# Kernel tuning notes

Hardware: AMD Instinct MI355X
Metric: run time of the kernel (lower is better)

The kernel has to match this reference:

```python
import jax, jax.numpy as jnp
import numpy as np

N, D, A, K, E = 8192, 256, 1024, 65, 4096

def setup_inputs() -> dict:
    key = jax.random.key(0)
    ks = jax.random.split(key, 8)
    s = 0.02  # linear-init scale to keep activations sane
    return {
        "embedding": jax.random.normal(ks[0], (N, D), jnp.float32),
        "data": jax.random.randint(ks[1], (E, 2), 0, N, jnp.int64),
        "Wq": jax.random.normal(ks[2], (D, A), jnp.float32) * s,
        "bq": jnp.zeros((A,), jnp.float32),
        "Wk": jax.random.normal(ks[3], (D, A), jnp.float32) * s,
        "bk": jnp.zeros((A,), jnp.float32),
        "Wv": jax.random.normal(ks[4], (D, A), jnp.float32) * s,
        "bv": jnp.zeros((A,), jnp.float32),
        "W_edge": jax.random.normal(ks[5], (K, A, A), jnp.float32) * s,
    }

def reference(embedding, data, Wq, bq, Wk, bk, Wv, bv, W_edge):
    # NodeSelfAttention: dense full attention over all N nodes
    Q = embedding @ Wq + bq            # [N, A]
    Km = embedding @ Wk + bk           # [N, A]
    V = embedding @ Wv + bv            # [N, A]
    scale = 1.0 / jnp.sqrt(jnp.float32(D))  # note: sqrt(num_feats)=sqrt(256), as in source
    scores = (Q @ Km.T) * scale        # [N, N]
    attn = jax.nn.softmax(scores, axis=-1)
    attn_emb = attn @ V                # [N, A]
    # gather edge endpoints
    h_u = attn_emb[data[:, 0]]         # [E, A]
    h_v = attn_emb[data[:, 1]]         # [E, A]
    # KWayPred: out[e,k] = h_u[e] @ W_edge[k] @ h_v[e]
    # (source computes full ExE matmul per k and takes diag; this is the
    #  equivalent O(E*K*A^2) bilinear-diag form)
    t = jnp.einsum('ed,kdf->ekf', h_u, W_edge)   # [E, K, A]
    out = jnp.einsum('ekf,ef->ek', t, h_v)       # [E, K]
    return out
```

## Files before the change

kernel.cpp:

```cpp
#include <hip/hip_runtime.h>
#include <cstdio>
#include <cstdint>

#define NTOK 8192
#define DIM  256
#define AA   1024
#define KE   65
#define EE   4096

typedef unsigned short u16;
typedef __attribute__((ext_vector_type(4))) float   f32x4;
typedef __attribute__((ext_vector_type(8))) short   bf16x8;
typedef __attribute__((ext_vector_type(8))) unsigned short u16x8;

#define DEVI __device__ __forceinline__

DEVI u16 f2bf(float f) {
  union { float f; unsigned u; } x; x.f = f;
  unsigned r = x.u + 0x7FFFu + ((x.u >> 16) & 1u);
  return (u16)(r >> 16);
}
DEVI float bf2f(u16 h) {
  union { unsigned u; float f; } x; x.u = ((unsigned)h) << 16;
  return x.f;
}

DEVI void gload16(const void* g, void* l) {
  __builtin_amdgcn_global_load_lds(
      (const __attribute__((address_space(1))) void*)g,
      (__attribute__((address_space(3))) void*)l,
      16, 0, 0);
}

DEVI void barx() {
  asm volatile("" ::: "memory");
  __builtin_amdgcn_s_barrier();
  asm volatile("" ::: "memory");
}

DEVI void stage_half(const u16* __restrict__ g0, int ld, char* dst, int tid) {
#pragma unroll
  for (int rr = 0; rr < 2; ++rr) {
    int o = rr * 8192 + (tid >> 6) * 1024 + (tid & 63) * 16;
    int q = o ^ (((o >> 7) & 7) << 4);
    gload16(g0 + (size_t)(q >> 7) * ld + ((q & 127) >> 1),
            dst + rr * 8192 + (tid >> 6) * 1024);
  }
}

template<int EPI, int QMODE>
__global__ __launch_bounds__(512, 2)
void gemm8(const u16* __restrict__ A, int lda,
           const u16* __restrict__ B, int ldb,
           int MT, int NT, int K,
           u16* __restrict__ o_s, float scale, int ldc,
           const u16* __restrict__ Hu, float* __restrict__ o_e,
           int* __restrict__ qcnt)
{
  __shared__ __align__(16) char lds[131072];
  __shared__ int s_idx;
  char* ldsA = lds;
  char* ldsB = lds + 65536;

  const int tid = threadIdx.x, lane = tid & 63, wave = tid >> 6;
  const int wm = (wave >> 2) * 128;
  const int wn = (wave & 3) * 64;
  const int wnl = (wave & 1) * 64;
  const int KT = K >> 6, KT2 = KT >> 1;
  const int r15 = lane & 15, g16 = (lane >> 4) << 4;

  int xcc;
  asm volatile("s_getreg_b32 %0, hwreg(20, 0, 32)" : "=s"(xcc));
  xcc &= 7;
  const int MPX = MT >> 3;
  const int NQ = NT >> 3, NR = NT & 7;

  const char* Ab_e = ldsA +         (wm >> 7) * 16384;
  const char* Ab_o = ldsA + 32768 + (wm >> 7) * 16384;
  const char* Bb_e = ldsB +         (wn >> 7) * 16384;
  const char* Bb_o = ldsB + 32768 + (wn >> 7) * 16384;

#define STAGE_A(tk, h) stage_half(A + (size_t)(m0 + (h)*128) * lda + (size_t)(tk)*64, lda, \
                                  ldsA + ((tk)&1) * 32768 + (h) * 16384, tid)
#define STAGE_B(tk, h) stage_half(B + (size_t)(n0 + (h)*128) * ldb + (size_t)(tk)*64, ldb, \
                                  ldsB + ((tk)&1) * 32768 + (h) * 16384, tid)
#define RD_A4(base, q) \
  _Pragma("unroll") for (int m = (q)*4; m < (q)*4+4; ++m) \
  _Pragma("unroll") for (int kk = 0; kk < 2; ++kk) { \
    int p = (m*16 + r15)*128 + kk*64 + g16; p ^= ((p>>7)&7)<<4; \
    a[m][kk] = *(const bf16x8*)((base) + p); }
#define RD_B2(base, q) \
  _Pragma("unroll") for (int n = (q)*2; n < (q)*2+2; ++n) \
  _Pragma("unroll") for (int kk = 0; kk < 2; ++kk) { \
    int p = (wnl + n*16 + r15)*128 + kk*64 + g16; p ^= ((p>>7)&7)<<4; \
    b[n][kk] = *(const bf16x8*)((base) + p); }
#define MM(QM, QN) do { \
  __builtin_amdgcn_s_setprio(1); \
  _Pragma("unroll") for (int kk = 0; kk < 2; ++kk) \
  _Pragma("unroll") for (int m = 0; m < 4; ++m) \
  _Pragma("unroll") for (int n = 0; n < 2; ++n) \
    acc[(QM)*4+m][(QN)*2+n] = __builtin_amdgcn_mfma_f32_16x16x32_bf16( \
        a[(QM)*4+m][kk], b[(QN)*2+n][kk], acc[(QM)*4+m][(QN)*2+n], 0, 0, 0); \
  __builtin_amdgcn_s_setprio(0); } while (0)
#define WAIT_LGKM0 do { asm volatile("s_waitcnt lgkmcnt(0)" ::: "memory"); \
                        __builtin_amdgcn_sched_barrier(0); } while (0)

  for (int dx = 0; dx < 8; ++dx) {
    const int qi = (xcc + dx) & 7;
    int per, nt_base = 0, nt_cnt = 0;
    if constexpr (QMODE == 0) {
      per = (MT * NT) >> 3;
    } else {
      nt_cnt  = NQ + (qi < NR ? 1 : 0);
      nt_base = qi * NQ + (qi < NR ? qi : NR);
      per     = nt_cnt * MT;
    }
    while (true) {
      if (tid == 0) s_idx = atomicAdd(&qcnt[qi], 1);
      __syncthreads();
      const int idx = s_idx;
      __syncthreads();
      if (idx >= per) break;
      int mt, nt;
      if constexpr (QMODE == 0) {
        mt = qi * MPX + (idx % MPX);
        nt = idx / MPX;
      } else {
        const int srw = nt_cnt << 3;
        const int sr  = idx / srw;
        const int rem = idx - sr * srw;
        nt = nt_base + (rem >> 3);
        mt = (sr << 3) + (rem & 7);
      }
      const int m0 = mt * 256, n0 = nt * 256;

      f32x4 acc[8][4];
#pragma unroll
      for (int m = 0; m < 8; ++m)
#pragma unroll
        for (int n = 0; n < 4; ++n) acc[m][n] = f32x4{0.f, 0.f, 0.f, 0.f};

      STAGE_A(0, 0); STAGE_A(0, 1); STAGE_B(0, 0); STAGE_B(0, 1);
      STAGE_A(1, 0); STAGE_B(1, 0);
      asm volatile("s_waitcnt vmcnt(4)" ::: "memory");
      barx();

      for (int i = 0; i < KT2; ++i) {
        const int ta = 2 * i, tb = 2 * i + 1;
        const bool lastI = (i == KT2 - 1);
        bf16x8 a[8][2], b[4][2];

        RD_B2(Bb_e, 0); RD_A4(Ab_e, 0);
        STAGE_A(tb, 1);
        asm volatile("s_waitcnt lgkmcnt(8)" ::: "memory");
        barx(); WAIT_LGKM0;
        MM(0, 0);
        barx();
        RD_B2(Bb_e, 1);
        STAGE_B(tb, 1);
        barx(); WAIT_LGKM0;
        MM(0, 1);
        barx();
        RD_A4(Ab_e, 1);
        if (!lastI) STAGE_B(ta + 2, 0);
        barx(); WAIT_LGKM0;
        MM(1, 1);
        barx();
        if (!lastI) STAGE_A(ta + 2, 0);
        barx();
        __builtin_amdgcn_sched_barrier(0);
        MM(1, 0);
        if (!lastI) asm volatile("s_waitcnt vmcnt(4)" ::: "memory");
        else        asm volatile("s_waitcnt vmcnt(0)" ::: "memory");
        barx();

        RD_B2(Bb_o, 0); RD_A4(Ab_o, 0);
        if (!lastI) STAGE_A(ta + 2, 1);
        asm volatile("s_waitcnt lgkmcnt(8)" ::: "memory");
        barx(); WAIT_LGKM0;
        MM(0, 0);
        barx();
        RD_B2(Bb_o, 1);
        if (!lastI) STAGE_B(ta + 2, 1);
        barx(); WAIT_LGKM0;
        MM(0, 1);
        barx();
        RD_A4(Ab_o, 1);
        if (!lastI) STAGE_B(tb + 2, 0);
        barx(); WAIT_LGKM0;
        MM(1, 1);
        barx();
        if (!lastI) STAGE_A(tb + 2, 0);
        barx();
        __builtin_amdgcn_sched_barrier(0);
        MM(1, 0);
        if (!lastI) asm volatile("s_waitcnt vmcnt(4)" ::: "memory");
        else        asm volatile("s_waitcnt vmcnt(0)" ::: "memory");
        barx();
      }

      const int rgrp = lane >> 4, cid = lane & 15;
      if constexpr (EPI == 1) {
#pragma unroll
        for (int m = 0; m < 8; ++m)
#pragma unroll
          for (int n = 0; n < 4; ++n)
#pragma unroll
            for (int j = 0; j < 4; ++j) {
              int row = m0 + wm + m * 16 + rgrp * 4 + j;
              int col = n0 + wn + n * 16 + cid;
              o_s[(size_t)row * ldc + col] = f2bf(acc[m][n][j] * scale);
            }
      } else {
        const int kidx  = n0 >> 10;
        const int dbase = (n0 & 1023) + wn;
#pragma unroll
        for (int m = 0; m < 8; ++m)
#pragma unroll
          for (int j = 0; j < 4; ++j) {
            int row = m0 + wm + m * 16 + rgrp * 4 + j;
            float p = 0.f;
#pragma unroll
            for (int n = 0; n < 4; ++n)
              p += acc[m][n][j] * bf2f(Hu[(size_t)row * AA + dbase + n * 16 + cid]);
            p += __shfl_xor(p, 1, 64);
            p += __shfl_xor(p, 2, 64);
            p += __shfl_xor(p, 4, 64);
            p += __shfl_xor(p, 8, 64);
            if (cid == 0) atomicAdd(&o_e[(size_t)row * KE + kidx], p);
          }
      }
    }
  }
#undef STAGE_A
#undef STAGE_B
#undef RD_A4
#undef RD_B2
#undef MM
#undef WAIT_LGKM0
}

#define BM 128
#define BN 128
#define BK 64

template<int EPI, bool BF32>
__global__ __launch_bounds__(256)
void gemm_bt(const u16* __restrict__ A, int lda,
             const void* __restrict__ Bptr, int ldb,
             int MT, int NT, int K,
             u16* __restrict__ o_q, u16* __restrict__ o_k, u16* __restrict__ o_vt,
             const float* __restrict__ biasc,
             u16* __restrict__ o_s, float scale, int ldc,
             const u16* __restrict__ Hu, float* __restrict__ o_e)
{
  const int nb  = MT * NT;
  const int per = nb >> 3;
  int bid = blockIdx.x;
  bid = (bid & 7) * per + (bid >> 3);
  const int mt = bid % MT, nt = bid / MT;
  const int m0 = mt * BM, n0 = nt * BN;

  __shared__ u16 As[BM * BK];
  __shared__ u16 Bs[BN * BK];

  const int tid  = threadIdx.x;
  const int lane = tid & 63, wave = tid >> 6;
  const int wm = (wave >> 1) * 64, wn = (wave & 1) * 64;

  f32x4 acc[4][4];
#pragma unroll
  for (int m = 0; m < 4; ++m)
#pragma unroll
    for (int n = 0; n < 4; ++n) acc[m][n] = f32x4{0.f, 0.f, 0.f, 0.f};

  const u16*   Bh = (const u16*)Bptr;
  const float* Bf = (const float*)Bptr;

  const int KT = K / BK;
  for (int kt = 0; kt < KT; ++kt) {
    const int k0 = kt * BK;
#pragma unroll
    for (int it = 0; it < 4; ++it) {
      int o = it * 4096 + wave * 1024 + lane * 16;
      int r = o >> 7;
      int c = (o & 127) >> 1;
      gload16(A + (size_t)(m0 + r) * lda + k0 + c,
              &As[(it * 4096 + wave * 1024) >> 1]);
    }
    if constexpr (!BF32) {
#pragma unroll
      for (int it = 0; it < 4; ++it) {
        int o = it * 4096 + wave * 1024 + lane * 16;
        int r = o >> 7;
        int c = (o & 127) >> 1;
        gload16(Bh + (size_t)(n0 + r) * ldb + k0 + c,
                &Bs[(it * 4096 + wave * 1024) >> 1]);
      }
    } else {
#pragma unroll
      for (int it = 0; it < 8; ++it) {
        int e = it * 1024 + tid * 4;
        int r = e >> 6, c = e & 63;
        const float4 v = *(const float4*)(Bf + (size_t)(n0 + r) * ldb + k0 + c);
        ushort4 h;
        h.x = f2bf(v.x); h.y = f2bf(v.y); h.z = f2bf(v.z); h.w = f2bf(v.w);
        *(ushort4*)&Bs[r * BK + c] = h;
      }
    }
    asm volatile("s_waitcnt vmcnt(0)" ::: "memory");
    __syncthreads();

#pragma unroll
    for (int kk = 0; kk < 2; ++kk) {
      const int ro = lane & 15;
      const int ko = kk * 32 + (lane >> 4) * 8;
      bf16x8 af[4], bfg[4];
#pragma unroll
      for (int m = 0; m < 4; ++m)
        af[m] = *(const bf16x8*)&As[(wm + m * 16 + ro) * BK + ko];
#pragma unroll
      for (int n = 0; n < 4; ++n)
        bfg[n] = *(const bf16x8*)&Bs[(wn + n * 16 + ro) * BK + ko];
#pragma unroll
      for (int m = 0; m < 4; ++m)
#pragma unroll
        for (int n = 0; n < 4; ++n)
          acc[m][n] = __builtin_amdgcn_mfma_f32_16x16x32_bf16(
              af[m], bfg[n], acc[m][n], 0, 0, 0);
    }
    __syncthreads();
  }

  const int rgrp = lane >> 4, cid = lane & 15;

  if constexpr (EPI == 0) {
#pragma unroll
    for (int m = 0; m < 4; ++m)
#pragma unroll
      for (int n = 0; n < 4; ++n)
#pragma unroll
        for (int j = 0; j < 4; ++j) {
          int row = m0 + wm + m * 16 + rgrp * 4 + j;
          int col = n0 + wn + n * 16 + cid;
          float v = acc[m][n][j] + biasc[col];
          u16 h = f2bf(v);
          if (col < 1024)       o_q[(size_t)row * AA + col] = h;
          else if (col < 2048)  o_k[(size_t)row * AA + (col - 1024)] = h;
          else                  o_vt[(size_t)(col - 2048) * NTOK + row] = h;
        }
  } else if constexpr (EPI == 1) {
#pragma unroll
    for (int m = 0; m < 4; ++m)
#pragma unroll
      for (int n = 0; n < 4; ++n)
#pragma unroll
        for (int j = 0; j < 4; ++j) {
          int row = m0 + wm + m * 16 + rgrp * 4 + j;
          int col = n0 + wn + n * 16 + cid;
          o_s[(size_t)row * ldc + col] = f2bf(acc[m][n][j] * scale);
        }
  } else {
    const int kidx  = n0 >> 10;
    const int dbase = (n0 & 1023) + wn;
#pragma unroll
    for (int m = 0; m < 4; ++m)
#pragma unroll
      for (int j = 0; j < 4; ++j) {
        int row = m0 + wm + m * 16 + rgrp * 4 + j;
        float p = 0.f;
#pragma unroll
        for (int n = 0; n < 4; ++n) {
          int d = dbase + n * 16 + cid;
          p += acc[m][n][j] * bf2f(Hu[(size_t)row * AA + d]);
        }
        p += __shfl_xor(p, 1, 64);
        p += __shfl_xor(p, 2, 64);
        p += __shfl_xor(p, 4, 64);
        p += __shfl_xor(p, 8, 64);
        if (cid == 0) atomicAdd(&o_e[(size_t)row * KE + kidx], p);
      }
  }
}

__global__ __launch_bounds__(256)
void softmax_rows(u16* __restrict__ S)
{
  const size_t base = (size_t)blockIdx.x * 8192;
  const int tid = threadIdx.x;
  const int lane = tid & 63, wave = tid >> 6;
  float v[32];
#pragma unroll
  for (int c = 0; c < 4; ++c) {
    u16x8 u = *(const u16x8*)&S[base + c * 2048 + tid * 8];
#pragma unroll
    for (int j = 0; j < 8; ++j) v[c * 8 + j] = bf2f(u[j]);
  }
  float mx = -1e30f;
#pragma unroll
  for (int i = 0; i < 32; ++i) mx = fmaxf(mx, v[i]);
#pragma unroll
  for (int off = 1; off < 64; off <<= 1) mx = fmaxf(mx, __shfl_xor(mx, off, 64));
  __shared__ float r1[4], r2[4];
  if (lane == 0) r1[wave] = mx;
  __syncthreads();
  mx = fmaxf(fmaxf(r1[0], r1[1]), fmaxf(r1[2], r1[3]));

  float s = 0.f;
#pragma unroll
  for (int i = 0; i < 32; ++i) { v[i] = __expf(v[i] - mx); s += v[i]; }
#pragma unroll
  for (int off = 1; off < 64; off <<= 1) s += __shfl_xor(s, off, 64);
  if (lane == 0) r2[wave] = s;
  __syncthreads();
  s = r2[0] + r2[1] + r2[2] + r2[3];
  const float inv = 1.f / s;
#pragma unroll
  for (int c = 0; c < 4; ++c) {
    u16x8 u;
#pragma unroll
    for (int j = 0; j < 8; ++j) u[j] = f2bf(v[c * 8 + j] * inv);
    *(u16x8*)&S[base + c * 2048 + tid * 8] = u;
  }
}

__global__ __launch_bounds__(256)
void gather_rows(const unsigned* __restrict__ dw, const u16* __restrict__ AE,
                 u16* __restrict__ Hu, u16* __restrict__ Hv)
{
  bool i64 = true;
#pragma unroll
  for (int w = 1; w < 32; w += 2) i64 = i64 && (dw[w] == 0u);
  const int e = blockIdx.x;
  const unsigned iu = i64 ? dw[4 * e]     : dw[2 * e];
  const unsigned iv = i64 ? dw[4 * e + 2] : dw[2 * e + 1];
  const int t = threadIdx.x;
  *(ushort4*)&Hu[(size_t)e * AA + t * 4] = *(const ushort4*)&AE[(size_t)iu * AA + t * 4];
  *(ushort4*)&Hv[(size_t)e * AA + t * 4] = *(const ushort4*)&AE[(size_t)iv * AA + t * 4];
}

__global__ __launch_bounds__(256)
void init_misc(float* __restrict__ out_e, const float* __restrict__ bq,
               const float* __restrict__ bk, const float* __restrict__ bv,
               float* __restrict__ biasc, int* __restrict__ qall)
{
  const int i = blockIdx.x * 256 + threadIdx.x;
  if (i < EE * KE) out_e[i] = 0.f;
  if (i < 1024) {
    biasc[i]        = bq[i];
    biasc[1024 + i] = bk[i];
    biasc[2048 + i] = bv[i];
  }
  if (i < 24) qall[i] = 0;
}

__global__ __launch_bounds__(256)
void cvt_f32_bf16_v4(const float* __restrict__ src, u16* __restrict__ dst, int n4)
{
  for (int i = blockIdx.x * 256 + threadIdx.x; i < n4; i += gridDim.x * 256) {
    float4 v = ((const float4*)src)[i];
    ushort4 h; h.x = f2bf(v.x); h.y = f2bf(v.y); h.z = f2bf(v.z); h.w = f2bf(v.w);
    ((ushort4*)dst)[i] = h;
  }
}

__global__ __launch_bounds__(256)
void build_wT(const float* __restrict__ Wq, const float* __restrict__ Wk,
              const float* __restrict__ Wv, u16* __restrict__ WT)
{
  const int nn = blockIdx.x;
  const int d  = threadIdx.x;
  const float* W = (nn < 1024) ? Wq : ((nn < 2048) ? Wk : Wv);
  WT[nn * DIM + d] = f2bf(W[(size_t)d * AA + (nn & 1023)]);
}

extern "C" void kernel_launch(void* const* d_in, const int* in_sizes, int n_in,
                              void* d_out, int out_size, void* d_ws, size_t ws_size,
                              hipStream_t stream)
{
  (void)in_sizes; (void)out_size;
  if (n_in < 9) return;
  const float*    emb  = (const float*)d_in[0];
  const unsigned* data = (const unsigned*)d_in[1];
  const float* Wq = (const float*)d_in[2];
  const float* bq = (const float*)d_in[3];
  const float* Wk = (const float*)d_in[4];
  const float* bk = (const float*)d_in[5];
  const float* Wv = (const float*)d_in[6];
  const float* bv = (const float*)d_in[7];
  const float* We = (const float*)d_in[8];
  float* out = (float*)d_out;

  char* ws = (char*)d_ws;
  size_t off = 0;
  auto alloc = [&](size_t bytes) -> void* {
    void* p = ws + off;
    off += (bytes + 255) & ~(size_t)255;
    return p;
  };
  u16*   emb_b = (u16*)alloc((size_t)NTOK * DIM * 2);
  u16*   WT    = (u16*)alloc((size_t)3072 * DIM * 2);
  float* biasc = (float*)alloc(3072 * 4);
  int*   qall  = (int*)alloc(24 * 4);
  u16*   Qb    = (u16*)alloc((size_t)NTOK * AA * 2);
  u16*   Kb    = (u16*)alloc((size_t)NTOK * AA * 2);
  u16*   Vt    = (u16*)alloc((size_t)AA * NTOK * 2);
  u16*   AE    = (u16*)alloc((size_t)NTOK * AA * 2);
  u16*   Hu    = (u16*)alloc((size_t)EE * AA * 2);
  u16*   Hv    = (u16*)alloc((size_t)EE * AA * 2);

  const size_t webf_bytes = ((size_t)KE * AA * AA * 2 + 255) & ~(size_t)255;
  u16* We_b = nullptr;
  if (off + webf_bytes + (size_t)1024 * NTOK * 2 <= ws_size) {
    We_b = (u16*)(ws + off);
    off += webf_bytes;
  }

  int chunk = 4096;
  while (chunk > 128 && off + (size_t)chunk * NTOK * 2 > ws_size) chunk >>= 1;
  u16* Sc = (u16*)alloc((size_t)chunk * NTOK * 2);
  if (off > ws_size) {
    fprintf(stderr, "kernel_launch: ws too small (need %zu, have %zu)\n", off, ws_size);
    return;
  }

  init_misc<<<(EE * KE) / 256, 256, 0, stream>>>(out, bq, bk, bv, biasc, qall);
  cvt_f32_bf16_v4<<<2048, 256, 0, stream>>>(emb, emb_b, NTOK * DIM / 4);
  build_wT<<<3072, 256, 0, stream>>>(Wq, Wk, Wv, WT);
  if (We_b)
    cvt_f32_bf16_v4<<<4096, 256, 0, stream>>>(We, We_b, KE * AA * AA / 4);

  gemm_bt<0, false><<<64 * 24, 256, 0, stream>>>(
      emb_b, DIM, WT, DIM, 64, 24, DIM,
      Qb, Kb, Vt, biasc, nullptr, 0.f, 0, nullptr, nullptr);

  const int nch = NTOK / chunk;
  for (int ci = 0; ci < nch; ++ci) {
    const u16* Qc = Qb + (size_t)ci * chunk * AA;
    if ((chunk & 2047) == 0)
      gemm8<1, 1><<<256, 512, 0, stream>>>(
          Qc, AA, Kb, AA, chunk / 256, 32, AA,
          Sc, 0.0625f, NTOK, nullptr, nullptr, qall + 8 * (ci & 1));
    else
      gemm_bt<1, false><<<(chunk / 128) * 64, 256, 0, stream>>>(
          Qc, AA, Kb, AA, chunk / 128, 64, AA,
          nullptr, nullptr, nullptr, nullptr, Sc, 0.0625f, NTOK, nullptr, nullptr);
    softmax_rows<<<chunk, 256, 0, stream>>>(Sc);
    gemm_bt<1, false><<<(chunk / 128) * 8, 256, 0, stream>>>(
        Sc, NTOK, Vt, NTOK, chunk / 128, 8, NTOK,
        nullptr, nullptr, nullptr, nullptr,
        AE + (size_t)ci * chunk * AA, 1.0f, AA, nullptr, nullptr);
  }

  gather_rows<<<EE, 256, 0, stream>>>(data, AE, Hu, Hv);

  if (We_b)
    gemm8<2, 1><<<256, 512, 0, stream>>>(
        Hv, AA, We_b, AA, 16, 260, AA,
        nullptr, 0.f, 0, Hu, out, qall + 16);
  else
    gemm_bt<3, true><<<32 * 520, 256, 0, stream>>>(
        Hv, AA, We, AA, 32, 520, AA,
        nullptr, nullptr, nullptr, nullptr, nullptr, 0.f, 0, Hu, out);
}
```

Before: 1.729 ms.

## Prefetch next tile across persistent gemm8 tiles and use gemm8 for attn@V

The persistent gemm8 kernel now pops its next tile index early, during the second-to-last K iteration, and starts staging that tile's first K slices while the current tile finishes. This removes the prologue bubble and the double __syncthreads between tiles. The K loop is restructured into a KTILE macro with deeper prefetch (vmcnt 6). The attn@V GEMM also switches from gemm_bt to gemm8 when the chunk is big, using QMODE 0, which needs separate queue counters per chunk. The cost is a more complex pipeline, with a risk of LDS races and higher register pressure.

Result: faster. 1.620 ms (-6.3%).

```diff
diff --git a/kernel.cpp b/kernel.cpp
--- a/kernel.cpp
+++ b/kernel.cpp
@@ -58,7 +58,7 @@
            int* __restrict__ qcnt)
 {
   __shared__ __align__(16) char lds[131072];
-  __shared__ int s_idx;
+  __shared__ int s_next[3];
   char* ldsA = lds;
   char* ldsB = lds + 65536;
 
@@ -80,10 +80,51 @@
   const char* Bb_e = ldsB +         (wn >> 7) * 16384;
   const char* Bb_o = ldsB + 32768 + (wn >> 7) * 16384;
 
-#define STAGE_A(tk, h) stage_half(A + (size_t)(m0 + (h)*128) * lda + (size_t)(tk)*64, lda, \
-                                  ldsA + ((tk)&1) * 32768 + (h) * 16384, tid)
-#define STAGE_B(tk, h) stage_half(B + (size_t)(n0 + (h)*128) * ldb + (size_t)(tk)*64, ldb, \
-                                  ldsB + ((tk)&1) * 32768 + (h) * 16384, tid)
+  int dxr = 0;
+  auto pop_next = [&]() {
+    while (dxr < 8) {
+      const int qi = (xcc + dxr) & 7;
+      int per, ntb = 0, ntc = 0;
+      if constexpr (QMODE == 0) {
+        per = (MT * NT) >> 3;
+      } else {
+        ntc = NQ + (qi < NR ? 1 : 0);
+        ntb = qi * NQ + (qi < NR ? qi : NR);
+        per = ntc * MT;
+      }
+      const int idx = atomicAdd(&qcnt[qi], 1);
+      if (idx < per) {
+        int mt, nt;
+        if constexpr (QMODE == 0) {
+          mt = qi * MPX + (idx % MPX); nt = idx / MPX;
+        } else {
+          const int srw = ntc << 3;
+          const int sr = idx / srw, rem = idx - sr * srw;
+          nt = ntb + (rem >> 3); mt = (sr << 3) + (rem & 7);
+        }
+        s_next[0] = mt * 256; s_next[1] = nt * 256; s_next[2] = 1;
+        return;
+      }
+      ++dxr;
+    }
+    s_next[2] = 0;
+  };
+
+  if (tid == 0) pop_next();
+  __syncthreads();
+  int m0 = s_next[0], n0 = s_next[1];
+  if (!s_next[2]) return;
+
+#define STAGE_A2(tk, h) do { const int _tk = (tk); \
+    if (_tk < KT) stage_half(A + (size_t)(m0 + (h)*128) * lda + (size_t)_tk*64, lda, \
+                             ldsA + (_tk & 1) * 32768 + (h) * 16384, tid); \
+    else if (have_n) stage_half(A + (size_t)(m0n + (h)*128) * lda + (size_t)(_tk-KT)*64, lda, \
+                                ldsA + (_tk & 1) * 32768 + (h) * 16384, tid); } while (0)
+#define STAGE_B2(tk, h) do { const int _tk = (tk); \
+    if (_tk < KT) stage_half(B + (size_t)(n0 + (h)*128) * ldb + (size_t)_tk*64, ldb, \
+                             ldsB + (_tk & 1) * 32768 + (h) * 16384, tid); \
+    else if (have_n) stage_half(B + (size_t)(n0n + (h)*128) * ldb + (size_t)(_tk-KT)*64, ldb, \
+                                ldsB + (_tk & 1) * 32768 + (h) * 16384, tid); } while (0)
 #define RD_A4(base, q) \
   _Pragma("unroll") for (int m = (q)*4; m < (q)*4+4; ++m) \
   _Pragma("unroll") for (int kk = 0; kk < 2; ++kk) { \
@@ -104,140 +145,106 @@
   __builtin_amdgcn_s_setprio(0); } while (0)
 #define WAIT_LGKM0 do { asm volatile("s_waitcnt lgkmcnt(0)" ::: "memory"); \
                         __builtin_amdgcn_sched_barrier(0); } while (0)
-
-  for (int dx = 0; dx < 8; ++dx) {
-    const int qi = (xcc + dx) & 7;
-    int per, nt_base = 0, nt_cnt = 0;
-    if constexpr (QMODE == 0) {
-      per = (MT * NT) >> 3;
-    } else {
-      nt_cnt  = NQ + (qi < NR ? 1 : 0);
-      nt_base = qi * NQ + (qi < NR ? qi : NR);
-      per     = nt_cnt * MT;
+#define KTILE(t, AB, BB) do { \
+     \
+    RD_B2(BB, 0); RD_A4(AB, 0); \
+    STAGE_B2((t) + 1, 1); \
+    asm volatile("s_waitcnt lgkmcnt(8)" ::: "memory"); \
+    barx(); WAIT_LGKM0; \
+    MM(0, 0); \
+    barx(); \
+     \
+    RD_B2(BB, 1); \
+    barx(); WAIT_LGKM0; \
+    MM(0, 1); \
+    barx(); \
+     \
+    RD_A4(AB, 1); \
+    STAGE_B2((t) + 2, 0); \
+    barx(); WAIT_LGKM0; \
+    MM(1, 1); \
+    barx(); \
+     \
+    STAGE_A2((t) + 2, 0); \
+    STAGE_A2((t) + 2, 1); \
+    barx(); \
+    __builtin_amdgcn_sched_barrier(0); \
+    MM(1, 0); \
+    if (vm6) asm volatile("s_waitcnt vmcnt(6)" ::: "memory"); \
+    else     asm volatile("s_waitcnt vmcnt(0)" ::: "memory"); \
+    barx(); } while (0)
+
+  {
+    const int m0n = 0, n0n = 0; const bool have_n = false; (void)m0n; (void)n0n; (void)have_n;
+    STAGE_A2(0, 0); STAGE_A2(0, 1); STAGE_B2(0, 0); STAGE_B2(0, 1);
+    STAGE_B2(1, 0); STAGE_A2(1, 0); STAGE_A2(1, 1);
+  }
+  asm volatile("s_waitcnt vmcnt(6)" ::: "memory");
+  barx();
+
+  while (true) {
+    f32x4 acc[8][4];
+#pragma unroll
+    for (int m = 0; m < 8; ++m)
+#pragma unroll
+      for (int n = 0; n < 4; ++n) acc[m][n] = f32x4{0.f, 0.f, 0.f, 0.f};
+
+    int m0n = 0, n0n = 0;
+    bool have_n = false;
+
+    for (int i = 0; i < KT2; ++i) {
+      const int ta = 2 * i, tb = 2 * i + 1;
+      if (i == KT2 - 2 && tid == 0) pop_next();
+      if (i == KT2 - 1) { m0n = s_next[0]; n0n = s_next[1]; have_n = (s_next[2] != 0); }
+      const bool tail = (i == KT2 - 1);
+      const bool vm6 = !tail || have_n;
+      bf16x8 a[8][2], b[4][2];
+      KTILE(ta, Ab_e, Bb_e);
+      KTILE(tb, Ab_o, Bb_o);
     }
-    while (true) {
-      if (tid == 0) s_idx = atomicAdd(&qcnt[qi], 1);
-      __syncthreads();
-      const int idx = s_idx;
-      __syncthreads();
-      if (idx >= per) break;
-      int mt, nt;
-      if constexpr (QMODE == 0) {
-        mt = qi * MPX + (idx % MPX);
-        nt = idx / MPX;
-      } else {
-        const int srw = nt_cnt << 3;
-        const int sr  = idx / srw;
-        const int rem = idx - sr * srw;
-        nt = nt_base + (rem >> 3);
-        mt = (sr << 3) + (rem & 7);
-      }
-      const int m0 = mt * 256, n0 = nt * 256;
-
-      f32x4 acc[8][4];
+
+    const int rgrp = lane >> 4, cid = lane & 15;
+    if constexpr (EPI == 1) {
 #pragma unroll
       for (int m = 0; m < 8; ++m)
 #pragma unroll
-        for (int n = 0; n < 4; ++n) acc[m][n] = f32x4{0.f, 0.f, 0.f, 0.f};
-
-      STAGE_A(0, 0); STAGE_A(0, 1); STAGE_B(0, 0); STAGE_B(0, 1);
-      STAGE_A(1, 0); STAGE_B(1, 0);
-      asm volatile("s_waitcnt vmcnt(4)" ::: "memory");
-      barx();
-
-      for (int i = 0; i < KT2; ++i) {
-        const int ta = 2 * i, tb = 2 * i + 1;
-        const bool lastI = (i == KT2 - 1);
-        bf16x8 a[8][2], b[4][2];
-
-        RD_B2(Bb_e, 0); RD_A4(Ab_e, 0);
-        STAGE_A(tb, 1);
-        asm volatile("s_waitcnt lgkmcnt(8)" ::: "memory");
-        barx(); WAIT_LGKM0;
-        MM(0, 0);
-        barx();
-        RD_B2(Bb_e, 1);
-        STAGE_B(tb, 1);
-        barx(); WAIT_LGKM0;
-        MM(0, 1);
-        barx();
-        RD_A4(Ab_e, 1);
-        if (!lastI) STAGE_B(ta + 2, 0);
-        barx(); WAIT_LGKM0;
-        MM(1, 1);
-        barx();
-        if (!lastI) STAGE_A(ta + 2, 0);
-        barx();
-        __builtin_amdgcn_sched_barrier(0);
-        MM(1, 0);
-        if (!lastI) asm volatile("s_waitcnt vmcnt(4)" ::: "memory");
-        else        asm volatile("s_waitcnt vmcnt(0)" ::: "memory");
-        barx();
-
-        RD_B2(Bb_o, 0); RD_A4(Ab_o, 0);
-        if (!lastI) STAGE_A(ta + 2, 1);
-        asm volatile("s_waitcnt lgkmcnt(8)" ::: "memory");
-        barx(); WAIT_LGKM0;
-        MM(0, 0);
-        barx();
-        RD_B2(Bb_o, 1);
-        if (!lastI) STAGE_B(ta + 2, 1);
-        barx(); WAIT_LGKM0;
-        MM(0, 1);
-        barx();
-        RD_A4(Ab_o, 1);
-        if (!lastI) STAGE_B(tb + 2, 0);
-        barx(); WAIT_LGKM0;
-        MM(1, 1);
-        barx();
-        if (!lastI) STAGE_A(tb + 2, 0);
-        barx();
-        __builtin_amdgcn_sched_barrier(0);
-        MM(1, 0);
-        if (!lastI) asm volatile("s_waitcnt vmcnt(4)" ::: "memory");
-        else        asm volatile("s_waitcnt vmcnt(0)" ::: "memory");
-        barx();
-      }
-
-      const int rgrp = lane >> 4, cid = lane & 15;
-      if constexpr (EPI == 1) {
-#pragma unroll
-        for (int m = 0; m < 8; ++m)
-#pragma unroll
-          for (int n = 0; n < 4; ++n)
-#pragma unroll
-            for (int j = 0; j < 4; ++j) {
-              int row = m0 + wm + m * 16 + rgrp * 4 + j;
-              int col = n0 + wn + n * 16 + cid;
-              o_s[(size_t)row * ldc + col] = f2bf(acc[m][n][j] * scale);
-            }
-      } else {
-        const int kidx  = n0 >> 10;
-        const int dbase = (n0 & 1023) + wn;
-#pragma unroll
-        for (int m = 0; m < 8; ++m)
+        for (int n = 0; n < 4; ++n)
 #pragma unroll
           for (int j = 0; j < 4; ++j) {
             int row = m0 + wm + m * 16 + rgrp * 4 + j;
-            float p = 0.f;
-#pragma unroll
-            for (int n = 0; n < 4; ++n)
-              p += acc[m][n][j] * bf2f(Hu[(size_t)row * AA + dbase + n * 16 + cid]);
-            p += __shfl_xor(p, 1, 64);
-            p += __shfl_xor(p, 2, 64);
-            p += __shfl_xor(p, 4, 64);
-            p += __shfl_xor(p, 8, 64);
-            if (cid == 0) atomicAdd(&o_e[(size_t)row * KE + kidx], p);
+            int col = n0 + wn + n * 16 + cid;
+            o_s[(size_t)row * ldc + col] = f2bf(acc[m][n][j] * scale);
           }
-      }
+    } else {
+      const int kidx  = n0 >> 10;
+      const int dbase = (n0 & 1023) + wn;
+#pragma unroll
+      for (int m = 0; m < 8; ++m)
+#pragma unroll
+        for (int j = 0; j < 4; ++j) {
+          int row = m0 + wm + m * 16 + rgrp * 4 + j;
+          float p = 0.f;
+#pragma unroll
+          for (int n = 0; n < 4; ++n)
+            p += acc[m][n][j] * bf2f(Hu[(size_t)row * AA + dbase + n * 16 + cid]);
+          p += __shfl_xor(p, 1, 64);
+          p += __shfl_xor(p, 2, 64);
+          p += __shfl_xor(p, 4, 64);
+          p += __shfl_xor(p, 8, 64);
+          if (cid == 0) atomicAdd(&o_e[(size_t)row * KE + kidx], p);
+        }
     }
-  }
-#undef STAGE_A
-#undef STAGE_B
+
+    if (!have_n) break;
+    m0 = m0n; n0 = n0n;
+  }
+#undef STAGE_A2
+#undef STAGE_B2
 #undef RD_A4
 #undef RD_B2
 #undef MM
 #undef WAIT_LGKM0
+#undef KTILE
 }
 
 #define BM 128
@@ -451,7 +458,7 @@
     biasc[1024 + i] = bk[i];
     biasc[2048 + i] = bv[i];
   }
-  if (i < 24) qall[i] = 0;
+  if (i < 64) qall[i] = 0;
 }
 
 __global__ __launch_bounds__(256)
@@ -501,7 +508,7 @@
   u16*   emb_b = (u16*)alloc((size_t)NTOK * DIM * 2);
   u16*   WT    = (u16*)alloc((size_t)3072 * DIM * 2);
   float* biasc = (float*)alloc(3072 * 4);
-  int*   qall  = (int*)alloc(24 * 4);
+  int*   qall  = (int*)alloc(64 * 4);
   u16*   Qb    = (u16*)alloc((size_t)NTOK * AA * 2);
   u16*   Kb    = (u16*)alloc((size_t)NTOK * AA * 2);
   u16*   Vt    = (u16*)alloc((size_t)AA * NTOK * 2);
@@ -537,19 +544,25 @@
   const int nch = NTOK / chunk;
   for (int ci = 0; ci < nch; ++ci) {
     const u16* Qc = Qb + (size_t)ci * chunk * AA;
-    if ((chunk & 2047) == 0)
+    const bool big = ((chunk & 2047) == 0);
+    if (big)
       gemm8<1, 1><<<256, 512, 0, stream>>>(
           Qc, AA, Kb, AA, chunk / 256, 32, AA,
-          Sc, 0.0625f, NTOK, nullptr, nullptr, qall + 8 * (ci & 1));
+          Sc, 0.0625f, NTOK, nullptr, nullptr, qall + 8 * ci);
     else
       gemm_bt<1, false><<<(chunk / 128) * 64, 256, 0, stream>>>(
           Qc, AA, Kb, AA, chunk / 128, 64, AA,
           nullptr, nullptr, nullptr, nullptr, Sc, 0.0625f, NTOK, nullptr, nullptr);
     softmax_rows<<<chunk, 256, 0, stream>>>(Sc);
-    gemm_bt<1, false><<<(chunk / 128) * 8, 256, 0, stream>>>(
-        Sc, NTOK, Vt, NTOK, chunk / 128, 8, NTOK,
-        nullptr, nullptr, nullptr, nullptr,
-        AE + (size_t)ci * chunk * AA, 1.0f, AA, nullptr, nullptr);
+    if (big)
+      gemm8<1, 0><<<256, 512, 0, stream>>>(
+          Sc, NTOK, Vt, NTOK, chunk / 256, 4, NTOK,
+          AE + (size_t)ci * chunk * AA, 1.0f, AA, nullptr, nullptr, qall + 16 + 8 * ci);
+    else
+      gemm_bt<1, false><<<(chunk / 128) * 8, 256, 0, stream>>>(
+          Sc, NTOK, Vt, NTOK, chunk / 128, 8, NTOK,
+          nullptr, nullptr, nullptr, nullptr,
+          AE + (size_t)ci * chunk * AA, 1.0f, AA, nullptr, nullptr);
   }
 
   gather_rows<<<EE, 256, 0, stream>>>(data, AE, Hu, Hv);
@@ -557,7 +570,7 @@
   if (We_b)
     gemm8<2, 1><<<256, 512, 0, stream>>>(
         Hv, AA, We_b, AA, 16, 260, AA,
-        nullptr, 0.f, 0, Hu, out, qall + 16);
+        nullptr, 0.f, 0, Hu, out, qall + 32);
   else
     gemm_bt<3, true><<<32 * 520, 256, 0, stream>>>(
         Hv, AA, We, AA, 32, 520, AA,
```
